# Optimization experiments

Measured on AMD Instinct MI355X. Metric: run time of the kernel, lower is better.

## Reference

```python
import jax, jax.numpy as jnp
import numpy as np
import math

B, S, D, H = 4, 512, 128, 4
HD = D // H
NEG = float(-2**32 + 1)

def _ln(x, g, b, eps=1e-8):
    m = jnp.mean(x, axis=-1, keepdims=True)
    v = jnp.var(x, axis=-1, keepdims=True)
    return (x - m) * jax.lax.rsqrt(v + eps) * g + b

def setup_inputs() -> dict:
    key = jax.random.key(0)
    ks = jax.random.split(key, 16)
    s = 0.02
    inp = {
        'embed': jax.random.normal(ks[0], (B, S, D), jnp.float32),
        'time_matrix_K': jax.random.normal(ks[1], (B, S, S, D), jnp.float32),
        'time_matrix_V': jax.random.normal(ks[2], (B, S, S, D), jnp.float32),
        # causal additive mask: large negative above diagonal (1--mask semantics)
        'attn_mask': jnp.where(jnp.triu(jnp.ones((S, S), bool), k=1), jnp.float32(-1e9), jnp.float32(0.0)),
        'padding_mask': jnp.zeros((B, S), bool),
        'wq': jax.random.normal(ks[3], (D, D), jnp.float32) * s,
        'bq': jnp.zeros((D,), jnp.float32),
        'wk': jax.random.normal(ks[4], (D, D), jnp.float32) * s,
        'bk': jnp.zeros((D,), jnp.float32),
        'wv': jax.random.normal(ks[5], (D, D), jnp.float32) * s,
        'bv': jnp.zeros((D,), jnp.float32),
        'wo': jax.random.normal(ks[6], (D, D), jnp.float32) * s,
        'bo': jnp.zeros((D,), jnp.float32),
        'ln1_g': jnp.ones((D,), jnp.float32),
        'ln1_b': jnp.zeros((D,), jnp.float32),
        'ln2_g': jnp.ones((D,), jnp.float32),
        'ln2_b': jnp.zeros((D,), jnp.float32),
        'w1': jax.random.normal(ks[7], (D, D), jnp.float32) * s,  # d_ff defaults to d_model
        'b1': jnp.zeros((D,), jnp.float32),
        'w2': jax.random.normal(ks[8], (D, D), jnp.float32) * s,
        'b2': jnp.zeros((D,), jnp.float32),
    }
    return inp

def reference(embed, time_matrix_K, time_matrix_V, attn_mask, padding_mask,
              wq, bq, wk, bk, wv, bv, wo, bo,
              ln1_g, ln1_b, ln2_g, ln2_b, w1, b1, w2, b2):
    # Pre-LN on Q only (K, V take raw embed), per original block
    Qn = _ln(embed, ln1_g, ln1_b)
    q = (Qn @ wq + bq).reshape(B, S, H, HD).transpose(0, 2, 1, 3)      # bhqd
    k = (embed @ wk + bk).reshape(B, S, H, HD).transpose(0, 2, 1, 3)   # bhkd
    v = (embed @ wv + bv).reshape(B, S, H, HD).transpose(0, 2, 1, 3)   # bhkd
    tmK = time_matrix_K.reshape(B, S, S, H, HD).transpose(0, 3, 1, 2, 4)  # bhqkd
    tmV = time_matrix_V.reshape(B, S, S, H, HD).transpose(0, 3, 1, 2, 4)  # bhqkd
    scale = math.sqrt(HD)
    energy = jnp.einsum('bhqd,bhkd->bhqk', q, k)
    energy = energy + jnp.einsum('bhqkd,bhqd->bhqk', tmK, q)
    energy = energy / scale
    energy = energy + attn_mask[None, None]
    energy = jnp.where(padding_mask[:, None, None, :], jnp.float32(NEG), energy)
    attn = jax.nn.softmax(energy, axis=-1)  # dropout is identity in eval
    O = jnp.einsum('bhqk,bhkd->bhqd', attn, v)
    O = O + jnp.einsum('bhqk,bhqkd->bhqd', attn, tmV)
    O = O.transpose(0, 2, 1, 3).reshape(B, S, D)
    O = O @ wo + bo
    x = Qn + O                      # residual adds LN'd Q, per original code
    x = _ln(x, ln2_g, ln2_b)
    ff = jax.nn.gelu(x @ w1 + b1, approximate=False) @ w2 + b2
    return ff + x
```

## Files before the change

kernel.cpp:

```cpp
#include <hip/hip_runtime.h>
#include <math.h>

#define Bsz 4
#define Ssz 512
#define Dsz 128
#define Hsz 4
#define HDsz 32
#define KT 64
#define NT 8

typedef float floatx4 __attribute__((ext_vector_type(4)));

static __device__ __forceinline__ float4 ldnt4(const float* p) {
    floatx4 v = __builtin_nontemporal_load(reinterpret_cast<const floatx4*>(p));
    float4 r; r.x = v.x; r.y = v.y; r.z = v.z; r.w = v.w;
    return r;
}

__global__ __launch_bounds__(128) void k_pre(
    const float* __restrict__ embed,
    const float* __restrict__ wq, const float* __restrict__ bq,
    const float* __restrict__ wk, const float* __restrict__ bk,
    const float* __restrict__ wv, const float* __restrict__ bv,
    const float* __restrict__ g1, const float* __restrict__ b1,
    float* __restrict__ Qn, float* __restrict__ Qp,
    float* __restrict__ Kp, float* __restrict__ Vp)
{
    __shared__ float xs[4][128];
    __shared__ float qs[4][128];
    const int t = threadIdx.x;
    const int row0 = blockIdx.x * 4;
    const int r = t >> 5;
    const int c = t & 31;
    const int d4 = c << 2;

    const float4* e4 = (const float4*)(embed + (size_t)row0 * Dsz);
    float4 x4 = e4[r * 32 + c];

    float s = x4.x + x4.y + x4.z + x4.w;
    #pragma unroll
    for (int o = 1; o < 32; o <<= 1) s += __shfl_xor(s, o);
    const float m = s * (1.0f / 128.0f);

    const float dx0 = x4.x - m, dx1 = x4.y - m, dx2 = x4.z - m, dx3 = x4.w - m;
    float vs = dx0*dx0 + dx1*dx1 + dx2*dx2 + dx3*dx3;
    #pragma unroll
    for (int o = 1; o < 32; o <<= 1) vs += __shfl_xor(vs, o);
    const float rstd = rsqrtf(vs * (1.0f / 128.0f) + 1e-8f);

    const float4 g4 = *(const float4*)(g1 + d4);
    const float4 bb4 = *(const float4*)(b1 + d4);
    float4 qn4;
    qn4.x = dx0 * rstd * g4.x + bb4.x;
    qn4.y = dx1 * rstd * g4.y + bb4.y;
    qn4.z = dx2 * rstd * g4.z + bb4.z;
    qn4.w = dx3 * rstd * g4.w + bb4.w;

    xs[r][d4+0] = x4.x; xs[r][d4+1] = x4.y; xs[r][d4+2] = x4.z; xs[r][d4+3] = x4.w;
    qs[r][d4+0] = qn4.x; qs[r][d4+1] = qn4.y; qs[r][d4+2] = qn4.z; qs[r][d4+3] = qn4.w;
    *(float4*)(Qn + (size_t)(row0 + r) * Dsz + d4) = qn4;
    __syncthreads();

    float aq[4] = {0,0,0,0}, ak[4] = {0,0,0,0}, av[4] = {0,0,0,0};
    for (int d = 0; d < 128; ++d) {
        const float wqv = wq[d*128 + t];
        const float wkv = wk[d*128 + t];
        const float wvv = wv[d*128 + t];
        #pragma unroll
        for (int rr = 0; rr < 4; ++rr) {
            aq[rr] += qs[rr][d] * wqv;
            ak[rr] += xs[rr][d] * wkv;
            av[rr] += xs[rr][d] * wvv;
        }
    }
    const float bqv = bq[t], bkv = bk[t], bvv = bv[t];
    #pragma unroll
    for (int rr = 0; rr < 4; ++rr) {
        const size_t o = (size_t)(row0 + rr) * Dsz + t;
        Qp[o] = aq[rr] + bqv;
        Kp[o] = ak[rr] + bkv;
        Vp[o] = av[rr] + bvv;
    }
}

__global__ __launch_bounds__(256) void k_attn_tile(
    const float* __restrict__ tmK, const float* __restrict__ tmV,
    const float* __restrict__ Qp, const float* __restrict__ Kp,
    const float* __restrict__ Vp,
    float* __restrict__ Opart,
    float* __restrict__ ml)
{
    __shared__ float p_lds[Hsz][KT];
    __shared__ float qv[Dsz];
    __shared__ float red[8][32][4];

    const int id = blockIdx.x;
    const int b = id & 3;
    const int q = (id >> 2) & (Ssz - 1);
    const int tile = id >> 11;
    const int k0 = tile * KT;
    if (k0 > q) return;

    const int t = threadIdx.x;
    const int nr_full = q - k0 + 1;
    const int nr = nr_full > KT ? KT : nr_full;
    const size_t rowq = (size_t)(b * Ssz + q);

    if (t < 128) qv[t] = Qp[rowq * Dsz + t];
    __syncthreads();

    const int kk_off = t >> 5;
    const int c = t & 31;
    const int d4 = c << 2;
    const int h = c >> 3;

    const float4 q4 = *(const float4*)(qv + d4);
    const float* tmKb = tmK + (rowq * (size_t)Ssz + k0) * Dsz;
    const float* Kb   = Kp + ((size_t)b * Ssz + k0) * Dsz;
    const float inv_scale = 0.17677669529663687f;

    int kr = 0;
    for (; kr + 32 <= nr; kr += 32) {
        float4 a[4], kv[4];
        #pragma unroll
        for (int u = 0; u < 4; ++u) {
            const int kk = kr + kk_off + 8*u;
            a[u]  = ldnt4(tmKb + (size_t)kk * Dsz + d4);
            kv[u] = *(const float4*)(Kb + (size_t)kk * Dsz + d4);
        }
        #pragma unroll
        for (int u = 0; u < 4; ++u) {
            float val = q4.x*(a[u].x+kv[u].x) + q4.y*(a[u].y+kv[u].y)
                      + q4.z*(a[u].z+kv[u].z) + q4.w*(a[u].w+kv[u].w);
            val += __shfl_xor(val, 1);
            val += __shfl_xor(val, 2);
            val += __shfl_xor(val, 4);
            if ((c & 7) == 0) p_lds[h][kr + kk_off + 8*u] = val * inv_scale;
        }
    }
    for (; kr < nr; kr += 8) {
        const int kk = kr + kk_off;
        float val = 0.0f;
        if (kk < nr) {
            const float4 a  = ldnt4(tmKb + (size_t)kk * Dsz + d4);
            const float4 kv = *(const float4*)(Kb + (size_t)kk * Dsz + d4);
            val = q4.x*(a.x+kv.x) + q4.y*(a.y+kv.y) + q4.z*(a.z+kv.z) + q4.w*(a.w+kv.w);
        }
        val += __shfl_xor(val, 1);
        val += __shfl_xor(val, 2);
        val += __shfl_xor(val, 4);
        if ((c & 7) == 0 && kk < nr) p_lds[h][kk] = val * inv_scale;
    }
    __syncthreads();

    {
        const int hh = t >> 6;
        const int lane = t & 63;
        float mx = -INFINITY;
        if (lane < nr) mx = p_lds[hh][lane];
        #pragma unroll
        for (int o = 1; o < 64; o <<= 1) mx = fmaxf(mx, __shfl_xor(mx, o));
        float p = 0.0f;
        if (lane < nr) {
            p = __expf(p_lds[hh][lane] - mx);
            p_lds[hh][lane] = p;
        }
        float ssum = p;
        #pragma unroll
        for (int o = 1; o < 64; o <<= 1) ssum += __shfl_xor(ssum, o);
        if (lane == 0) {
            float* mlp = ml + ((rowq * NT + tile) * Hsz + hh) * 2;
            mlp[0] = mx;
            mlp[1] = ssum;
        }
    }
    __syncthreads();

    const float* tmVb = tmV + (rowq * (size_t)Ssz + k0) * Dsz;
    const float* Vb   = Vp + ((size_t)b * Ssz + k0) * Dsz;
    float4 acc = {0.0f, 0.0f, 0.0f, 0.0f};
    kr = 0;
    for (; kr + 32 <= nr; kr += 32) {
        float4 a[4], vv[4];
        #pragma unroll
        for (int u = 0; u < 4; ++u) {
            const int kk = kr + kk_off + 8*u;
            a[u]  = ldnt4(tmVb + (size_t)kk * Dsz + d4);
            vv[u] = *(const float4*)(Vb + (size_t)kk * Dsz + d4);
        }
        #pragma unroll
        for (int u = 0; u < 4; ++u) {
            const float p = p_lds[h][kr + kk_off + 8*u];
            acc.x += p * (a[u].x + vv[u].x);
            acc.y += p * (a[u].y + vv[u].y);
            acc.z += p * (a[u].z + vv[u].z);
            acc.w += p * (a[u].w + vv[u].w);
        }
    }
    for (; kr < nr; kr += 8) {
        const int kk = kr + kk_off;
        if (kk < nr) {
            const float p = p_lds[h][kk];
            const float4 a  = ldnt4(tmVb + (size_t)kk * Dsz + d4);
            const float4 vv = *(const float4*)(Vb + (size_t)kk * Dsz + d4);
            acc.x += p * (a.x + vv.x);
            acc.y += p * (a.y + vv.y);
            acc.z += p * (a.z + vv.z);
            acc.w += p * (a.w + vv.w);
        }
    }
    red[kk_off][c][0] = acc.x;
    red[kk_off][c][1] = acc.y;
    red[kk_off][c][2] = acc.z;
    red[kk_off][c][3] = acc.w;
    __syncthreads();
    if (t < 128) {
        const int cc = t >> 2, j = t & 3;
        float ssum = 0.0f;
        #pragma unroll
        for (int g = 0; g < 8; ++g) ssum += red[g][cc][j];
        Opart[(rowq * NT + tile) * Dsz + t] = ssum;
    }
}

__global__ __launch_bounds__(128) void k_combine(
    const float* __restrict__ Opart, const float* __restrict__ ml,
    float* __restrict__ Oa)
{
    const size_t rowq = blockIdx.x;
    const int q = (int)(rowq & (Ssz - 1));
    const int nt = (q >> 6) + 1;
    const int d = threadIdx.x;
    const int h = d >> 5;

    float M = -INFINITY;
    #pragma unroll 8
    for (int i = 0; i < nt; ++i)
        M = fmaxf(M, ml[((rowq * NT + i) * Hsz + h) * 2 + 0]);

    float den = 0.0f, o = 0.0f;
    #pragma unroll 8
    for (int i = 0; i < nt; ++i) {
        const float* mlp = ml + ((rowq * NT + i) * Hsz + h) * 2;
        const float w = __expf(mlp[0] - M);
        den += w * mlp[1];
        o   += w * Opart[(rowq * NT + i) * Dsz + d];
    }
    Oa[rowq * Dsz + d] = o / den;
}

__global__ __launch_bounds__(128) void k_post(
    const float* __restrict__ Oa, const float* __restrict__ Qn,
    const float* __restrict__ wo, const float* __restrict__ bo,
    const float* __restrict__ g2, const float* __restrict__ b2ln,
    const float* __restrict__ w1, const float* __restrict__ b1,
    const float* __restrict__ w2, const float* __restrict__ b2,
    float* __restrict__ out)
{
    __shared__ float os[4][128];
    __shared__ float xn[4][128];
    __shared__ float hbuf[4][128];
    const int t = threadIdx.x;
    const int row0 = blockIdx.x * 4;
    const int r = t >> 5;
    const int c = t & 31;
    const int d4 = c << 2;

    {
        const float4* o4 = (const float4*)(Oa + (size_t)row0 * Dsz);
        const float4 v = o4[r * 32 + c];
        os[r][d4+0] = v.x; os[r][d4+1] = v.y; os[r][d4+2] = v.z; os[r][d4+3] = v.w;
    }
    __syncthreads();

    float ao[4] = {0,0,0,0};
    for (int d = 0; d < 128; ++d) {
        const float wv = wo[d*128 + t];
        #pragma unroll
        for (int rr = 0; rr < 4; ++rr) ao[rr] += os[rr][d] * wv;
    }
    const float bov = bo[t];
    float xrow[4];
    #pragma unroll
    for (int rr = 0; rr < 4; ++rr)
        xrow[rr] = Qn[(size_t)(row0 + rr) * Dsz + t] + ao[rr] + bov;
    __syncthreads();
    #pragma unroll
    for (int rr = 0; rr < 4; ++rr) os[rr][t] = xrow[rr];
    __syncthreads();

    {
        const float4 x4 = *(const float4*)(&os[r][d4]);
        float s = x4.x + x4.y + x4.z + x4.w;
        #pragma unroll
        for (int o = 1; o < 32; o <<= 1) s += __shfl_xor(s, o);
        const float m = s * (1.0f / 128.0f);
        const float dx0 = x4.x - m, dx1 = x4.y - m, dx2 = x4.z - m, dx3 = x4.w - m;
        float vs = dx0*dx0 + dx1*dx1 + dx2*dx2 + dx3*dx3;
        #pragma unroll
        for (int o = 1; o < 32; o <<= 1) vs += __shfl_xor(vs, o);
        const float rstd = rsqrtf(vs * (1.0f / 128.0f) + 1e-8f);
        const float4 g4 = *(const float4*)(g2 + d4);
        const float4 bb4 = *(const float4*)(b2ln + d4);
        xn[r][d4+0] = dx0 * rstd * g4.x + bb4.x;
        xn[r][d4+1] = dx1 * rstd * g4.y + bb4.y;
        xn[r][d4+2] = dx2 * rstd * g4.z + bb4.z;
        xn[r][d4+3] = dx3 * rstd * g4.w + bb4.w;
    }
    __syncthreads();

    float a1[4] = {0,0,0,0};
    for (int d = 0; d < 128; ++d) {
        const float wv = w1[d*128 + t];
        #pragma unroll
        for (int rr = 0; rr < 4; ++rr) a1[rr] += xn[rr][d] * wv;
    }
    const float b1v = b1[t];
    #pragma unroll
    for (int rr = 0; rr < 4; ++rr) {
        const float hv = a1[rr] + b1v;
        hbuf[rr][t] = 0.5f * hv * (1.0f + erff(hv * 0.70710678118654752f));
    }
    __syncthreads();

    float a2[4] = {0,0,0,0};
    for (int d = 0; d < 128; ++d) {
        const float wv = w2[d*128 + t];
        #pragma unroll
        for (int rr = 0; rr < 4; ++rr) a2[rr] += hbuf[rr][d] * wv;
    }
    const float b2v = b2[t];
    #pragma unroll
    for (int rr = 0; rr < 4; ++rr)
        out[(size_t)(row0 + rr) * Dsz + t] = a2[rr] + b2v + xn[rr][t];
}

extern "C" void kernel_launch(void* const* d_in, const int* in_sizes, int n_in,
                              void* d_out, int out_size, void* d_ws, size_t ws_size,
                              hipStream_t stream) {
    const float* embed = (const float*)d_in[0];
    const float* tmK   = (const float*)d_in[1];
    const float* tmV   = (const float*)d_in[2];
    const float* wq = (const float*)d_in[5];
    const float* bq = (const float*)d_in[6];
    const float* wk = (const float*)d_in[7];
    const float* bk = (const float*)d_in[8];
    const float* wv = (const float*)d_in[9];
    const float* bv = (const float*)d_in[10];
    const float* wo = (const float*)d_in[11];
    const float* bo = (const float*)d_in[12];
    const float* g1 = (const float*)d_in[13];
    const float* b1l = (const float*)d_in[14];
    const float* g2 = (const float*)d_in[15];
    const float* b2l = (const float*)d_in[16];
    const float* w1 = (const float*)d_in[17];
    const float* b1 = (const float*)d_in[18];
    const float* w2 = (const float*)d_in[19];
    const float* b2 = (const float*)d_in[20];

    const size_t NE = (size_t)Bsz * Ssz * Dsz;
    float* ws = (float*)d_ws;
    float* Qn = ws;
    float* Qp = ws + NE;
    float* Kp = ws + 2 * NE;
    float* Vp = ws + 3 * NE;
    float* Oa = ws + 4 * NE;
    float* Opart = ws + 5 * NE;
    float* mlbuf = ws + 5 * NE + (size_t)Bsz * Ssz * NT * Dsz;

    k_pre<<<(Bsz * Ssz) / 4, 128, 0, stream>>>(embed, wq, bq, wk, bk, wv, bv,
                                               g1, b1l, Qn, Qp, Kp, Vp);
    k_attn_tile<<<Bsz * Ssz * NT, 256, 0, stream>>>(tmK, tmV, Qp, Kp, Vp,
                                                    Opart, mlbuf);
    k_combine<<<Bsz * Ssz, 128, 0, stream>>>(Opart, mlbuf, Oa);
    k_post<<<(Bsz * Ssz) / 4, 128, 0, stream>>>(Oa, Qn, wo, bo, g2, b2l,
                                                w1, b1, w2, b2, (float*)d_out);
}
```

Baseline: 144.6 us.

## Map one wavefront per head in attention tile, drop shared memory and barriers

Each of the four wavefronts in the attention tile block now owns one head. The scores, softmax and PV accumulation stay in registers, using wavefront shuffles in place of shared-memory staging and three block barriers. The 1/sqrt(d) scale is folded into Q in the projection kernel, so the attention kernel skips that multiply. The per-lane access pattern changes from full 512-byte rows per 32 lanes to 128-byte head slices per 8 lanes, which may affect how well the tmK/tmV streaming loads coalesce.

```diff
diff --git a/kernel.cpp b/kernel.cpp
--- a/kernel.cpp
+++ b/kernel.cpp
@@ -23,7 +23,7 @@
     const float* __restrict__ wk, const float* __restrict__ bk,
     const float* __restrict__ wv, const float* __restrict__ bv,
     const float* __restrict__ g1, const float* __restrict__ b1,
-    float* __restrict__ Qn, float* __restrict__ Qp,
+    float* __restrict__ Qn, float* __restrict__ Qs,
     float* __restrict__ Kp, float* __restrict__ Vp)
 {
     __shared__ float xs[4][128];
@@ -73,11 +73,12 @@
             av[rr] += xs[rr][d] * wvv;
         }
     }
+    const float inv_scale = 0.17677669529663687f;
     const float bqv = bq[t], bkv = bk[t], bvv = bv[t];
     #pragma unroll
     for (int rr = 0; rr < 4; ++rr) {
         const size_t o = (size_t)(row0 + rr) * Dsz + t;
-        Qp[o] = aq[rr] + bqv;
+        Qs[o] = (aq[rr] + bqv) * inv_scale;
         Kp[o] = ak[rr] + bkv;
         Vp[o] = av[rr] + bvv;
     }
@@ -85,15 +86,11 @@
 
 __global__ __launch_bounds__(256) void k_attn_tile(
     const float* __restrict__ tmK, const float* __restrict__ tmV,
-    const float* __restrict__ Qp, const float* __restrict__ Kp,
+    const float* __restrict__ Qs, const float* __restrict__ Kp,
     const float* __restrict__ Vp,
     float* __restrict__ Opart,
     float* __restrict__ ml)
 {
-    __shared__ float p_lds[Hsz][KT];
-    __shared__ float qv[Dsz];
-    __shared__ float red[8][32][4];
-
     const int id = blockIdx.x;
     const int b = id & 3;
     const int q = (id >> 2) & (Ssz - 1);
@@ -102,124 +99,104 @@
     if (k0 > q) return;
 
     const int t = threadIdx.x;
+    const int w = t >> 6;
+    const int lane = t & 63;
+    const int rg = lane >> 3;
+    const int fs = lane & 7;
+    const int d4 = w * HDsz + fs * 4;
+
     const int nr_full = q - k0 + 1;
     const int nr = nr_full > KT ? KT : nr_full;
     const size_t rowq = (size_t)(b * Ssz + q);
 
-    if (t < 128) qv[t] = Qp[rowq * Dsz + t];
-    __syncthreads();
-
-    const int kk_off = t >> 5;
-    const int c = t & 31;
-    const int d4 = c << 2;
-    const int h = c >> 3;
-
-    const float4 q4 = *(const float4*)(qv + d4);
+    const float4 q4 = *(const float4*)(Qs + rowq * Dsz + d4);
     const float* tmKb = tmK + (rowq * (size_t)Ssz + k0) * Dsz;
     const float* Kb   = Kp + ((size_t)b * Ssz + k0) * Dsz;
-    const float inv_scale = 0.17677669529663687f;
-
-    int kr = 0;
-    for (; kr + 32 <= nr; kr += 32) {
+
+    float p[8];
+    #pragma unroll
+    for (int i0 = 0; i0 < 8; i0 += 4) {
         float4 a[4], kv[4];
         #pragma unroll
         for (int u = 0; u < 4; ++u) {
-            const int kk = kr + kk_off + 8*u;
-            a[u]  = ldnt4(tmKb + (size_t)kk * Dsz + d4);
-            kv[u] = *(const float4*)(Kb + (size_t)kk * Dsz + d4);
+            const int r = (i0 + u) * 8 + rg;
+            if (r < nr) {
+                a[u]  = ldnt4(tmKb + (size_t)r * Dsz + d4);
+                kv[u] = *(const float4*)(Kb + (size_t)r * Dsz + d4);
+            } else {
+                a[u] = make_float4(0,0,0,0); kv[u] = make_float4(0,0,0,0);
+            }
         }
         #pragma unroll
         for (int u = 0; u < 4; ++u) {
+            const int r = (i0 + u) * 8 + rg;
             float val = q4.x*(a[u].x+kv[u].x) + q4.y*(a[u].y+kv[u].y)
                       + q4.z*(a[u].z+kv[u].z) + q4.w*(a[u].w+kv[u].w);
             val += __shfl_xor(val, 1);
             val += __shfl_xor(val, 2);
             val += __shfl_xor(val, 4);
-            if ((c & 7) == 0) p_lds[h][kr + kk_off + 8*u] = val * inv_scale;
-        }
-    }
-    for (; kr < nr; kr += 8) {
-        const int kk = kr + kk_off;
-        float val = 0.0f;
-        if (kk < nr) {
-            const float4 a  = ldnt4(tmKb + (size_t)kk * Dsz + d4);
-            const float4 kv = *(const float4*)(Kb + (size_t)kk * Dsz + d4);
-            val = q4.x*(a.x+kv.x) + q4.y*(a.y+kv.y) + q4.z*(a.z+kv.z) + q4.w*(a.w+kv.w);
-        }
-        val += __shfl_xor(val, 1);
-        val += __shfl_xor(val, 2);
-        val += __shfl_xor(val, 4);
-        if ((c & 7) == 0 && kk < nr) p_lds[h][kk] = val * inv_scale;
-    }
-    __syncthreads();
-
-    {
-        const int hh = t >> 6;
-        const int lane = t & 63;
-        float mx = -INFINITY;
-        if (lane < nr) mx = p_lds[hh][lane];
-        #pragma unroll
-        for (int o = 1; o < 64; o <<= 1) mx = fmaxf(mx, __shfl_xor(mx, o));
-        float p = 0.0f;
-        if (lane < nr) {
-            p = __expf(p_lds[hh][lane] - mx);
-            p_lds[hh][lane] = p;
-        }
-        float ssum = p;
-        #pragma unroll
-        for (int o = 1; o < 64; o <<= 1) ssum += __shfl_xor(ssum, o);
-        if (lane == 0) {
-            float* mlp = ml + ((rowq * NT + tile) * Hsz + hh) * 2;
-            mlp[0] = mx;
-            mlp[1] = ssum;
-        }
-    }
-    __syncthreads();
+            p[i0 + u] = (r < nr) ? val : -INFINITY;
+        }
+    }
+
+    float mx = p[0];
+    #pragma unroll
+    for (int i = 1; i < 8; ++i) mx = fmaxf(mx, p[i]);
+    mx = fmaxf(mx, __shfl_xor(mx, 8));
+    mx = fmaxf(mx, __shfl_xor(mx, 16));
+    mx = fmaxf(mx, __shfl_xor(mx, 32));
+
+    float lsum = 0.0f;
+    #pragma unroll
+    for (int i = 0; i < 8; ++i) {
+        p[i] = __expf(p[i] - mx);
+        lsum += p[i];
+    }
+    lsum += __shfl_xor(lsum, 8);
+    lsum += __shfl_xor(lsum, 16);
+    lsum += __shfl_xor(lsum, 32);
+
+    if (lane == 0) {
+        float* mlp = ml + ((rowq * NT + tile) * Hsz + w) * 2;
+        mlp[0] = mx;
+        mlp[1] = lsum;
+    }
 
     const float* tmVb = tmV + (rowq * (size_t)Ssz + k0) * Dsz;
     const float* Vb   = Vp + ((size_t)b * Ssz + k0) * Dsz;
     float4 acc = {0.0f, 0.0f, 0.0f, 0.0f};
-    kr = 0;
-    for (; kr + 32 <= nr; kr += 32) {
+    #pragma unroll
+    for (int i0 = 0; i0 < 8; i0 += 4) {
         float4 a[4], vv[4];
         #pragma unroll
         for (int u = 0; u < 4; ++u) {
-            const int kk = kr + kk_off + 8*u;
-            a[u]  = ldnt4(tmVb + (size_t)kk * Dsz + d4);
-            vv[u] = *(const float4*)(Vb + (size_t)kk * Dsz + d4);
+            const int r = (i0 + u) * 8 + rg;
+            if (r < nr) {
+                a[u]  = ldnt4(tmVb + (size_t)r * Dsz + d4);
+                vv[u] = *(const float4*)(Vb + (size_t)r * Dsz + d4);
+            } else {
+                a[u] = make_float4(0,0,0,0); vv[u] = make_float4(0,0,0,0);
+            }
         }
         #pragma unroll
         for (int u = 0; u < 4; ++u) {
-            const float p = p_lds[h][kr + kk_off + 8*u];
-            acc.x += p * (a[u].x + vv[u].x);
-            acc.y += p * (a[u].y + vv[u].y);
-            acc.z += p * (a[u].z + vv[u].z);
-            acc.w += p * (a[u].w + vv[u].w);
-        }
-    }
-    for (; kr < nr; kr += 8) {
-        const int kk = kr + kk_off;
-        if (kk < nr) {
-            const float p = p_lds[h][kk];
-            const float4 a  = ldnt4(tmVb + (size_t)kk * Dsz + d4);
-            const float4 vv = *(const float4*)(Vb + (size_t)kk * Dsz + d4);
-            acc.x += p * (a.x + vv.x);
-            acc.y += p * (a.y + vv.y);
-            acc.z += p * (a.z + vv.z);
-            acc.w += p * (a.w + vv.w);
-        }
-    }
-    red[kk_off][c][0] = acc.x;
-    red[kk_off][c][1] = acc.y;
-    red[kk_off][c][2] = acc.z;
-    red[kk_off][c][3] = acc.w;
-    __syncthreads();
-    if (t < 128) {
-        const int cc = t >> 2, j = t & 3;
-        float ssum = 0.0f;
-        #pragma unroll
-        for (int g = 0; g < 8; ++g) ssum += red[g][cc][j];
-        Opart[(rowq * NT + tile) * Dsz + t] = ssum;
+            const float pw = p[i0 + u];
+            acc.x += pw * (a[u].x + vv[u].x);
+            acc.y += pw * (a[u].y + vv[u].y);
+            acc.z += pw * (a[u].z + vv[u].z);
+            acc.w += pw * (a[u].w + vv[u].w);
+        }
+    }
+    #pragma unroll
+    for (int o = 8; o < 64; o <<= 1) {
+        acc.x += __shfl_xor(acc.x, o);
+        acc.y += __shfl_xor(acc.y, o);
+        acc.z += __shfl_xor(acc.z, o);
+        acc.w += __shfl_xor(acc.w, o);
+    }
+    if (lane < 8) {
+        float4* op = (float4*)(Opart + (rowq * NT + tile) * Dsz + d4);
+        *op = acc;
     }
 }
 
@@ -361,7 +338,7 @@
     const size_t NE = (size_t)Bsz * Ssz * Dsz;
     float* ws = (float*)d_ws;
     float* Qn = ws;
-    float* Qp = ws + NE;
+    float* Qs = ws + NE;
     float* Kp = ws + 2 * NE;
     float* Vp = ws + 3 * NE;
     float* Oa = ws + 4 * NE;
@@ -369,8 +346,8 @@
     float* mlbuf = ws + 5 * NE + (size_t)Bsz * Ssz * NT * Dsz;
 
     k_pre<<<(Bsz * Ssz) / 4, 128, 0, stream>>>(embed, wq, bq, wk, bk, wv, bv,
-                                               g1, b1l, Qn, Qp, Kp, Vp);
-    k_attn_tile<<<Bsz * Ssz * NT, 256, 0, stream>>>(tmK, tmV, Qp, Kp, Vp,
+                                               g1, b1l, Qn, Qs, Kp, Vp);
+    k_attn_tile<<<Bsz * Ssz * NT, 256, 0, stream>>>(tmK, tmV, Qs, Kp, Vp,
                                                     Opart, mlbuf);
     k_combine<<<Bsz * Ssz, 128, 0, stream>>>(Opart, mlbuf, Oa);
     k_post<<<(Bsz * Ssz) / 4, 128, 0, stream>>>(Oa, Qn, wo, bo, g2, b2l,
```

After: 141.6 us. -2.0%, faster.
